# Optimization experiments

Hardware: AMD Instinct MI355X
Metric: run time of the kernel (lower is better)

Reference implementation:

```python
import jax, jax.numpy as jnp
import numpy as np

N_NODES = 100000


def _gcn_layer(x, src, dst, deg_inv_sqrt, W, b):
    # GCNConv: out = D^{-1/2} (A + I) D^{-1/2} X W + b  (symmetric norm, self-loops)
    xw = x @ W  # [N, out]
    norm = deg_inv_sqrt[src] * deg_inv_sqrt[dst]  # [E]
    msg = xw[src] * norm[:, None]  # [E, out] gathered messages
    agg = jax.ops.segment_sum(msg, dst, num_segments=N_NODES)
    # self-loop contribution: norm_ii = deg_inv_sqrt[i]^2
    agg = agg + (deg_inv_sqrt * deg_inv_sqrt)[:, None] * xw
    return agg + b


def setup_inputs() -> dict:
    key = jax.random.key(0)
    k1, k2, k3, k4, k5, k6 = jax.random.split(key, 6)
    F_IN, HID, OUT, E = 128, 256, 40, 1600000
    x = jax.random.normal(k1, (N_NODES, F_IN), dtype=jnp.float32)
    edge_index = jax.random.randint(k2, (2, E), 0, N_NODES, dtype=jnp.int64)
    s1 = 1.0 / np.sqrt(F_IN)
    s2 = 1.0 / np.sqrt(HID)
    W1 = jax.random.uniform(k3, (F_IN, HID), jnp.float32, -s1, s1)
    b1 = jnp.zeros((HID,), jnp.float32)
    W2 = jax.random.uniform(k4, (HID, OUT), jnp.float32, -s2, s2)
    b2 = jnp.zeros((OUT,), jnp.float32)
    return {"x": x, "edge_index": edge_index, "W1": W1, "b1": b1, "W2": W2, "b2": b2}


def reference(x, edge_index, W1, b1, W2, b2):
    src, dst = edge_index[0], edge_index[1]
    # degree with self-loops (GCNConv default add_self_loops=True)
    deg = jax.ops.segment_sum(jnp.ones_like(dst, dtype=x.dtype), dst, num_segments=N_NODES) + 1.0
    deg_inv_sqrt = jax.lax.rsqrt(deg)
    h = _gcn_layer(x, src, dst, deg_inv_sqrt, W1, b1)
    h = jax.nn.relu(h)
    # dropout is identity in eval mode
    h = _gcn_layer(h, src, dst, deg_inv_sqrt, W2, b2)
    return jax.nn.log_softmax(h, axis=1)
```

## Files before the change

kernel.cpp:

```cpp
#include <hip/hip_runtime.h>
#include <math.h>

typedef long long ll;
typedef unsigned int uint;
typedef __attribute__((ext_vector_type(8))) short bf16x8;
typedef __attribute__((ext_vector_type(4))) float f32x4;

#define FIN 128
#define HID 256
#define FOUT 40
#define NG 8
#define NBIN 64

__device__ __forceinline__ float bflo(uint u) { return __uint_as_float(u << 16); }
__device__ __forceinline__ float bfhi(uint u) { return __uint_as_float(u & 0xFFFF0000u); }
__device__ __forceinline__ unsigned short f2bf(float f) {
  uint u = __float_as_uint(f);
  u += 0x7FFFu + ((u >> 16) & 1u);
  return (unsigned short)(u >> 16);
}

__device__ __forceinline__ int detect64(const uint* __restrict__ ei) {
  return (ei[1] == 0u && ei[3] == 0u && ei[5] == 0u && ei[7] == 0u) ? 1 : 0;
}

__global__ __launch_bounds__(256) void k_init(
    const void* __restrict__ ei, int* __restrict__ cnt,
    const float* __restrict__ W1, const float* __restrict__ W2,
    unsigned short* __restrict__ w1p, unsigned short* __restrict__ w2p,
    int2* __restrict__ pairs, ll E) {
  int i = blockIdx.x * 256 + threadIdx.x;
  int T = gridDim.x * 256;
  if (i < 32768) {
    int j = i & 7, g = (i >> 3) & 3, c = (i >> 5) & 255, s = i >> 13;
    int k = s * 32 + g * 8 + j;
    w1p[i] = f2bf(W1[(size_t)k * HID + c]);
  } else if (i < 32768 + 12288) {
    int i2 = i - 32768;
    int j = i2 & 7, g = (i2 >> 3) & 3, q = i2 >> 5;
    int c = q % 48, s = q / 48;
    int k = s * 32 + g * 8 + j;
    w2p[i2] = (c < FOUT) ? f2bf(W2[(size_t)k * FOUT + c]) : (unsigned short)0;
  }
  int is64 = detect64((const uint*)ei);
  for (ll base = (ll)i * 4; base < E; base += (ll)T * 4) {
    int m = (int)((E - base < 4) ? (E - base) : 4);
    int s[4], d[4];
    if (is64) {
      if (m == 4) {
        longlong2 a0 = *(const longlong2*)((const ll*)ei + base);
        longlong2 a1 = *(const longlong2*)((const ll*)ei + base + 2);
        longlong2 b0 = *(const longlong2*)((const ll*)ei + E + base);
        longlong2 b1 = *(const longlong2*)((const ll*)ei + E + base + 2);
        s[0]=(int)a0.x; s[1]=(int)a0.y; s[2]=(int)a1.x; s[3]=(int)a1.y;
        d[0]=(int)b0.x; d[1]=(int)b0.y; d[2]=(int)b1.x; d[3]=(int)b1.y;
      } else {
        for (int j = 0; j < m; ++j) { s[j]=(int)((const ll*)ei)[base+j]; d[j]=(int)((const ll*)ei)[E+base+j]; }
      }
    } else {
      if (m == 4) {
        int4 a = *(const int4*)((const int*)ei + base);
        int4 b = *(const int4*)((const int*)ei + E + base);
        s[0]=a.x; s[1]=a.y; s[2]=a.z; s[3]=a.w;
        d[0]=b.x; d[1]=b.y; d[2]=b.z; d[3]=b.w;
      } else {
        for (int j = 0; j < m; ++j) { s[j]=((const int*)ei)[base+j]; d[j]=((const int*)ei)[E+base+j]; }
      }
    }
    if (m == 4) {
      *(int4*)(pairs + base)     = make_int4(s[0], d[0], s[1], d[1]);
      *(int4*)(pairs + base + 2) = make_int4(s[2], d[2], s[3], d[3]);
    } else {
      for (int j = 0; j < m; ++j) pairs[base + j] = make_int2(s[j], d[j]);
    }
    for (int j = 0; j < m; ++j) atomicAdd(&cnt[d[j]], 1);
  }
}

__global__ __launch_bounds__(1024) void k_scan1(const int* __restrict__ cnt,
                                                int* __restrict__ row_off,
                                                int* __restrict__ blksums, int n) {
  __shared__ int sm[1024];
  int t = threadIdx.x;
  int base = blockIdx.x * 4096 + t * 4;
  int v0 = (base + 0 < n) ? cnt[base + 0] : 0;
  int v1 = (base + 1 < n) ? cnt[base + 1] : 0;
  int v2 = (base + 2 < n) ? cnt[base + 2] : 0;
  int v3 = (base + 3 < n) ? cnt[base + 3] : 0;
  int s = v0 + v1 + v2 + v3;
  sm[t] = s;
  __syncthreads();
  for (int off = 1; off < 1024; off <<= 1) {
    int u = (t >= off) ? sm[t - off] : 0;
    __syncthreads();
    sm[t] += u;
    __syncthreads();
  }
  int excl = sm[t] - s;
  if (base + 0 < n) row_off[base + 0] = excl;
  if (base + 1 < n) row_off[base + 1] = excl + v0;
  if (base + 2 < n) row_off[base + 2] = excl + v0 + v1;
  if (base + 3 < n) row_off[base + 3] = excl + v0 + v1 + v2;
  if (t == 1023) blksums[blockIdx.x] = sm[1023];
}

__global__ void k_scan2(int* __restrict__ blksums, int nb) {
  if (threadIdx.x == 0 && blockIdx.x == 0) {
    int acc = 0;
    for (int i = 0; i < nb; ++i) { int v = blksums[i]; blksums[i] = acc; acc += v; }
    blksums[nb] = acc;
  }
}

__global__ __launch_bounds__(1024) void k_scan3(
    int* __restrict__ row_off, int* __restrict__ cursor,
    const int* __restrict__ blksums, float* __restrict__ dis,
    int* __restrict__ hist, int n, int nb) {
  __shared__ int lh[NBIN];
  int t = threadIdx.x;
  if (t < NBIN) lh[t] = 0;
  __syncthreads();
  int i = blockIdx.x * 1024 + t;
  if (i < n) {
    int c = cursor[i];
    int v = row_off[i] + blksums[i >> 12];
    row_off[i] = v;
    cursor[i] = v;
    dis[i] = rsqrtf((float)c + 1.0f);
    atomicAdd(&lh[min(c, NBIN - 1)], 1);
  }
  if (i == 0) row_off[n] = blksums[nb];
  __syncthreads();
  if (t < NBIN && lh[t]) atomicAdd(&hist[t], lh[t]);
}

__global__ void k_binpfx(const int* __restrict__ hist, int* __restrict__ bincur) {
  if (threadIdx.x == 0 && blockIdx.x == 0) {
    int acc = 0;
    for (int b = 0; b < NBIN; ++b) { int v = hist[b]; bincur[b] = acc; acc += v; }
  }
}

__global__ __launch_bounds__(256) void k_perm(
    const int* __restrict__ row_off, int* __restrict__ bincur,
    int* __restrict__ perm, int n) {
  __shared__ int lh[NBIN], lbase[NBIN];
  int t = threadIdx.x;
  if (t < NBIN) lh[t] = 0;
  __syncthreads();
  int base = blockIdx.x * 4096 + t * 16;
  int deg[16];
  #pragma unroll
  for (int j = 0; j < 16; ++j) {
    int i = base + j;
    if (i < n) {
      deg[j] = min(row_off[i + 1] - row_off[i], NBIN - 1);
      atomicAdd(&lh[deg[j]], 1);
    } else deg[j] = -1;
  }
  __syncthreads();
  if (t < NBIN) {
    lbase[t] = lh[t] ? atomicAdd(&bincur[t], lh[t]) : 0;
    lh[t] = 0;
  }
  __syncthreads();
  #pragma unroll
  for (int j = 0; j < 16; ++j) {
    if (deg[j] >= 0) {
      int r = atomicAdd(&lh[deg[j]], 1);
      perm[lbase[deg[j]] + r] = base + j;
    }
  }
}

__global__ __launch_bounds__(256) void k_fill(
    const int2* __restrict__ pairs, int* __restrict__ cursor,
    int* __restrict__ csr, ll E, int range, int n) {
  int g = blockIdx.x & (NG - 1);
  int lo = g * range;
  int hi = min(n, lo + range);
  ll tig = (ll)(blockIdx.x >> 3) * 256 + threadIdx.x;
  ll TIG = (ll)(gridDim.x >> 3) * 256;
  for (ll i = tig * 2; i < E; i += TIG * 2) {
    if (i + 1 < E) {
      int4 p = *(const int4*)(pairs + i);
      if (p.y >= lo && p.y < hi) { int pos = atomicAdd(&cursor[p.y], 1); csr[pos] = p.x; }
      if (p.w >= lo && p.w < hi) { int pos = atomicAdd(&cursor[p.w], 1); csr[pos] = p.z; }
    } else {
      int2 p = pairs[i];
      if (p.y >= lo && p.y < hi) { int pos = atomicAdd(&cursor[p.y], 1); csr[pos] = p.x; }
    }
  }
}

__global__ __launch_bounds__(256) void k_xcast(
    const float* __restrict__ x, const float* __restrict__ dis,
    unsigned short* __restrict__ xb, int total8) {
  int i = blockIdx.x * 256 + threadIdx.x;
  if (i >= total8) return;
  float w = dis[i >> 4];
  const float4* p = (const float4*)x + (size_t)i * 2;
  float4 a = p[0], b = p[1];
  uint4 o;
  o.x = (uint)f2bf(w * a.x) | ((uint)f2bf(w * a.y) << 16);
  o.y = (uint)f2bf(w * a.z) | ((uint)f2bf(w * a.w) << 16);
  o.z = (uint)f2bf(w * b.x) | ((uint)f2bf(w * b.y) << 16);
  o.w = (uint)f2bf(w * b.z) | ((uint)f2bf(w * b.w) << 16);
  *(uint4*)(xb + (size_t)i * 8) = o;
}

__device__ __forceinline__ void add8(float* a, uint4 r) {
  a[0] += bflo(r.x); a[1] += bfhi(r.x);
  a[2] += bflo(r.y); a[3] += bfhi(r.y);
  a[4] += bflo(r.z); a[5] += bfhi(r.z);
  a[6] += bflo(r.w); a[7] += bfhi(r.w);
}

__global__ __launch_bounds__(256) void k_fused1(
    const unsigned short* __restrict__ xb, const int* __restrict__ csr,
    const int* __restrict__ row_off, const float* __restrict__ dis,
    const int* __restrict__ perm,
    const unsigned short* __restrict__ w1p, const float* __restrict__ b1,
    const unsigned short* __restrict__ w2p, unsigned short* __restrict__ xw2b,
    int n)
{
  __shared__ __align__(16) unsigned short xsb[16 * 136];
  __shared__ __align__(16) unsigned short hsb[16 * 264];
  __shared__ int   nid[16];
  __shared__ float dsh[16];

  int tid = threadIdx.x;
  int n0 = blockIdx.x * 16;
  int wv = tid >> 6, lane = tid & 63, qq = lane >> 4, l16 = lane & 15;
  int nl = wv * 4 + qq;
  int idx = n0 + nl;
  int node = (idx < n) ? perm[idx] : -1;

  float a[8] = {0, 0, 0, 0, 0, 0, 0, 0};
  float di = 0.f;
  if (node >= 0) {
    di = dis[node];
    uint4 v = *((const uint4*)(xb + (size_t)node * FIN) + l16);
    add8(a, v);
    int e0 = row_off[node], e1 = row_off[node + 1];
    int e = e0;
    for (; e + 8 <= e1; e += 8) {
      int s0 = csr[e],     s1 = csr[e + 1], s2 = csr[e + 2], s3 = csr[e + 3];
      int s4 = csr[e + 4], s5 = csr[e + 5], s6 = csr[e + 6], s7 = csr[e + 7];
      uint4 r0 = *((const uint4*)(xb + (size_t)s0 * FIN) + l16);
      uint4 r1 = *((const uint4*)(xb + (size_t)s1 * FIN) + l16);
      uint4 r2 = *((const uint4*)(xb + (size_t)s2 * FIN) + l16);
      uint4 r3 = *((const uint4*)(xb + (size_t)s3 * FIN) + l16);
      uint4 r4 = *((const uint4*)(xb + (size_t)s4 * FIN) + l16);
      uint4 r5 = *((const uint4*)(xb + (size_t)s5 * FIN) + l16);
      uint4 r6 = *((const uint4*)(xb + (size_t)s6 * FIN) + l16);
      uint4 r7 = *((const uint4*)(xb + (size_t)s7 * FIN) + l16);
      add8(a, r0); add8(a, r1); add8(a, r2); add8(a, r3);
      add8(a, r4); add8(a, r5); add8(a, r6); add8(a, r7);
    }
    for (; e < e1; ++e) {
      uint4 r0 = *((const uint4*)(xb + (size_t)csr[e] * FIN) + l16);
      add8(a, r0);
    }
  }
  if (l16 == 0) { nid[nl] = node; dsh[nl] = di; }
  {
    uint4 pk;
    pk.x = (uint)f2bf(di * a[0]) | ((uint)f2bf(di * a[1]) << 16);
    pk.y = (uint)f2bf(di * a[2]) | ((uint)f2bf(di * a[3]) << 16);
    pk.z = (uint)f2bf(di * a[4]) | ((uint)f2bf(di * a[5]) << 16);
    pk.w = (uint)f2bf(di * a[6]) | ((uint)f2bf(di * a[7]) << 16);
    *(uint4*)(xsb + nl * 136 + l16 * 8) = pk;
  }
  __syncthreads();

  int mrow = lane & 15, g = lane >> 4;
  f32x4 acc1[4] = {{0,0,0,0},{0,0,0,0},{0,0,0,0},{0,0,0,0}};
  #pragma unroll
  for (int s = 0; s < 4; ++s) {
    bf16x8 av = *(const bf16x8*)(xsb + mrow * 136 + s * 32 + g * 8);
    #pragma unroll
    for (int t = 0; t < 4; ++t) {
      int c = wv * 64 + t * 16 + mrow;
      bf16x8 bv = *(const bf16x8*)(w1p + (((size_t)(s * 256 + c) * 4 + g) << 3));
      acc1[t] = __builtin_amdgcn_mfma_f32_16x16x32_bf16(av, bv, acc1[t], 0, 0, 0);
    }
  }
  #pragma unroll
  for (int t = 0; t < 4; ++t) {
    int c = wv * 64 + t * 16 + mrow;
    float bb = b1[c];
    #pragma unroll
    for (int r = 0; r < 4; ++r) {
      float v = fmaxf(acc1[t][r] + bb, 0.f);
      hsb[(g * 4 + r) * 264 + c] = f2bf(v);
    }
  }
  __syncthreads();

  if (wv < 3) {
    f32x4 acc2 = {0, 0, 0, 0};
    int c2 = wv * 16 + mrow;
    #pragma unroll
    for (int s = 0; s < 8; ++s) {
      bf16x8 av = *(const bf16x8*)(hsb + mrow * 264 + s * 32 + g * 8);
      bf16x8 bv = *(const bf16x8*)(w2p + (((size_t)(s * 48 + c2) * 4 + g) << 3));
      acc2 = __builtin_amdgcn_mfma_f32_16x16x32_bf16(av, bv, acc2, 0, 0, 0);
    }
    if (c2 < FOUT) {
      #pragma unroll
      for (int r = 0; r < 4; ++r) {
        int nodeg = nid[g * 4 + r];
        if (nodeg >= 0)
          xw2b[(size_t)nodeg * FOUT + c2] = f2bf(acc2[r] * dsh[g * 4 + r]);
      }
    }
  }
}

__global__ __launch_bounds__(256) void k_layer2(
    const unsigned short* __restrict__ xw2b, const int* __restrict__ csr,
    const int* __restrict__ row_off, const float* __restrict__ dis,
    const int* __restrict__ perm,
    const float* __restrict__ b2, float* __restrict__ out, int n)
{
  int tid = threadIdx.x;
  int idx = blockIdx.x * 16 + (tid >> 4);
  int l16 = tid & 15;
  if (idx >= n) return;
  int node = perm[idx];
  float di = dis[node];
  bool act = (l16 < 10);
  float a0 = 0.f, a1 = 0.f, a2 = 0.f, a3 = 0.f;
  if (act) {
    uint2 v = *((const uint2*)(xw2b + (size_t)node * FOUT) + l16);
    a0 = bflo(v.x); a1 = bfhi(v.x); a2 = bflo(v.y); a3 = bfhi(v.y);
  }
  int e0 = row_off[node], e1 = row_off[node + 1];
  int e = e0;
  for (; e + 8 <= e1; e += 8) {
    int s0 = csr[e],     s1 = csr[e + 1], s2 = csr[e + 2], s3 = csr[e + 3];
    int s4 = csr[e + 4], s5 = csr[e + 5], s6 = csr[e + 6], s7 = csr[e + 7];
    if (act) {
      uint2 r0 = *((const uint2*)(xw2b + (size_t)s0 * FOUT) + l16);
      uint2 r1 = *((const uint2*)(xw2b + (size_t)s1 * FOUT) + l16);
      uint2 r2 = *((const uint2*)(xw2b + (size_t)s2 * FOUT) + l16);
      uint2 r3 = *((const uint2*)(xw2b + (size_t)s3 * FOUT) + l16);
      uint2 r4 = *((const uint2*)(xw2b + (size_t)s4 * FOUT) + l16);
      uint2 r5 = *((const uint2*)(xw2b + (size_t)s5 * FOUT) + l16);
      uint2 r6 = *((const uint2*)(xw2b + (size_t)s6 * FOUT) + l16);
      uint2 r7 = *((const uint2*)(xw2b + (size_t)s7 * FOUT) + l16);
      a0 += bflo(r0.x); a1 += bfhi(r0.x); a2 += bflo(r0.y); a3 += bfhi(r0.y);
      a0 += bflo(r1.x); a1 += bfhi(r1.x); a2 += bflo(r1.y); a3 += bfhi(r1.y);
      a0 += bflo(r2.x); a1 += bfhi(r2.x); a2 += bflo(r2.y); a3 += bfhi(r2.y);
      a0 += bflo(r3.x); a1 += bfhi(r3.x); a2 += bflo(r3.y); a3 += bfhi(r3.y);
      a0 += bflo(r4.x); a1 += bfhi(r4.x); a2 += bflo(r4.y); a3 += bfhi(r4.y);
      a0 += bflo(r5.x); a1 += bfhi(r5.x); a2 += bflo(r5.y); a3 += bfhi(r5.y);
      a0 += bflo(r6.x); a1 += bfhi(r6.x); a2 += bflo(r6.y); a3 += bfhi(r6.y);
      a0 += bflo(r7.x); a1 += bfhi(r7.x); a2 += bflo(r7.y); a3 += bfhi(r7.y);
    }
  }
  for (; e < e1; ++e) {
    int s0 = csr[e];
    if (act) {
      uint2 r0 = *((const uint2*)(xw2b + (size_t)s0 * FOUT) + l16);
      a0 += bflo(r0.x); a1 += bfhi(r0.x); a2 += bflo(r0.y); a3 += bfhi(r0.y);
    }
  }
  float l0 = -INFINITY, l1 = -INFINITY, l2 = -INFINITY, l3 = -INFINITY;
  if (act) {
    float4 bv = *(const float4*)(b2 + l16 * 4);
    l0 = di * a0 + bv.x; l1 = di * a1 + bv.y;
    l2 = di * a2 + bv.z; l3 = di * a3 + bv.w;
  }
  float m = fmaxf(fmaxf(l0, l1), fmaxf(l2, l3));
  #pragma unroll
  for (int off = 8; off > 0; off >>= 1) m = fmaxf(m, __shfl_xor(m, off));
  float s = 0.f;
  if (act) s = expf(l0 - m) + expf(l1 - m) + expf(l2 - m) + expf(l3 - m);
  #pragma unroll
  for (int off = 8; off > 0; off >>= 1) s += __shfl_xor(s, off);
  if (act) {
    float ls = m + logf(s);
    float4 o = make_float4(l0 - ls, l1 - ls, l2 - ls, l3 - ls);
    *(float4*)(out + (size_t)node * FOUT + l16 * 4) = o;
  }
}

extern "C" void kernel_launch(void* const* d_in, const int* in_sizes, int n_in,
                              void* d_out, int out_size, void* d_ws, size_t ws_size,
                              hipStream_t stream) {
  const float* x  = (const float*)d_in[0];
  const void*  ei = d_in[1];
  const float* W1 = (const float*)d_in[2];
  const float* b1 = (const float*)d_in[3];
  const float* W2 = (const float*)d_in[4];
  const float* b2 = (const float*)d_in[5];
  float* out = (float*)d_out;

  int n = in_sizes[0] / FIN;
  ll  E = (ll)in_sizes[1] / 2;
  int nb = (n + 4095) / 4096;
  int range = (n + NG - 1) / NG;

  char* ws = (char*)d_ws;
  size_t off = 0;
  auto carve = [&](size_t bytes) -> char* {
    char* p = ws + off;
    off = (off + bytes + 255) & ~(size_t)255;
    return p;
  };
  int*   row_off = (int*)carve((size_t)(n + 1) * 4);
  int*   cursor  = (int*)carve((size_t)n * 4);
  int2*  pairs   = (int2*)carve((size_t)E * 8);
  int*   csr     = (int*)carve((size_t)E * 4);
  int*   blksums = (int*)carve(64 * 4);
  int*   hist    = (int*)carve(NBIN * 4);
  int*   bincur  = (int*)carve(NBIN * 4);
  int*   perm    = (int*)carve((size_t)n * 4);
  float* dis     = (float*)carve((size_t)n * 4);
  unsigned short* xb   = (unsigned short*)carve((size_t)n * FIN * 2);
  unsigned short* w1p  = (unsigned short*)carve(32768 * 2);
  unsigned short* w2p  = (unsigned short*)carve(12288 * 2);
  unsigned short* xw2b = (unsigned short*)carve((size_t)n * FOUT * 2);
  (void)n_in; (void)out_size; (void)ws_size;

  int gx8  = (n * FIN / 8 + 255) / 256;
  int gt16 = (n + 15) / 16;
  int gperm = (n + 4095) / 4096;

  hipMemsetAsync(cursor, 0, (size_t)n * 4, stream);
  hipMemsetAsync(hist, 0, NBIN * 4, stream);

  hipLaunchKernelGGL(k_init,  dim3(2048), dim3(256), 0, stream,
                     ei, cursor, W1, W2, w1p, w2p, pairs, E);
  hipLaunchKernelGGL(k_scan1, dim3(nb), dim3(1024), 0, stream, cursor, row_off, blksums, n);
  hipLaunchKernelGGL(k_scan2, dim3(1), dim3(1), 0, stream, blksums, nb);
  hipLaunchKernelGGL(k_scan3, dim3((n + 1023) / 1024), dim3(1024), 0, stream,
                     row_off, cursor, blksums, dis, hist, n, nb);
  hipLaunchKernelGGL(k_binpfx, dim3(1), dim3(1), 0, stream, hist, bincur);
  hipLaunchKernelGGL(k_perm,  dim3(gperm), dim3(256), 0, stream, row_off, bincur, perm, n);
  hipLaunchKernelGGL(k_fill,  dim3(2048), dim3(256), 0, stream, pairs, cursor, csr, E, range, n);
  hipLaunchKernelGGL(k_xcast, dim3(gx8), dim3(256), 0, stream, x, dis, xb, n * FIN / 8);
  hipLaunchKernelGGL(k_fused1, dim3(gt16), dim3(256), 0, stream,
                     xb, csr, row_off, dis, perm, w1p, b1, w2p, xw2b, n);
  hipLaunchKernelGGL(k_layer2, dim3(gt16), dim3(256), 0, stream,
                     xw2b, csr, row_off, dis, perm, b2, out, n);
}
```

Before: 300.9 us.

## Split degree counting into range-partitioned pass and reverse block order in aggregation kernels

Degree counting moves out of k_init into a new k_count kernel. It re-reads the packed pairs and does its atomics only on destination nodes in one of two ranges per block group, so atomic traffic stays localized in cache. The fill kernel's partition count drops from 8 to 2. The fused layer-1 and layer-2 kernels now walk blocks in reverse order, so the highest-degree nodes in the permutation start first (load-balance tail). The cost is one extra kernel launch and a second full pass over the pairs array.

```diff
diff --git a/kernel.cpp b/kernel.cpp
--- a/kernel.cpp
+++ b/kernel.cpp
@@ -9,7 +9,7 @@
 #define FIN 128
 #define HID 256
 #define FOUT 40
-#define NG 8
+#define NGF 2
 #define NBIN 64
 
 __device__ __forceinline__ float bflo(uint u) { return __uint_as_float(u << 16); }
@@ -25,7 +25,7 @@
 }
 
 __global__ __launch_bounds__(256) void k_init(
-    const void* __restrict__ ei, int* __restrict__ cnt,
+    const void* __restrict__ ei,
     const float* __restrict__ W1, const float* __restrict__ W2,
     unsigned short* __restrict__ w1p, unsigned short* __restrict__ w2p,
     int2* __restrict__ pairs, ll E) {
@@ -73,7 +73,25 @@
     } else {
       for (int j = 0; j < m; ++j) pairs[base + j] = make_int2(s[j], d[j]);
     }
-    for (int j = 0; j < m; ++j) atomicAdd(&cnt[d[j]], 1);
+  }
+}
+
+__global__ __launch_bounds__(256) void k_count(
+    const int2* __restrict__ pairs, int* __restrict__ cnt, ll E, int range, int n) {
+  int g = blockIdx.x & (NGF - 1);
+  int lo = g * range;
+  int hi = min(n, lo + range);
+  ll tig = (ll)(blockIdx.x >> 1) * 256 + threadIdx.x;
+  ll TIG = (ll)(gridDim.x >> 1) * 256;
+  for (ll i = tig * 2; i < E; i += TIG * 2) {
+    if (i + 1 < E) {
+      int4 p = *(const int4*)(pairs + i);
+      if (p.y >= lo && p.y < hi) atomicAdd(&cnt[p.y], 1);
+      if (p.w >= lo && p.w < hi) atomicAdd(&cnt[p.w], 1);
+    } else {
+      int2 p = pairs[i];
+      if (p.y >= lo && p.y < hi) atomicAdd(&cnt[p.y], 1);
+    }
   }
 }
 
@@ -176,11 +194,11 @@
 __global__ __launch_bounds__(256) void k_fill(
     const int2* __restrict__ pairs, int* __restrict__ cursor,
     int* __restrict__ csr, ll E, int range, int n) {
-  int g = blockIdx.x & (NG - 1);
+  int g = blockIdx.x & (NGF - 1);
   int lo = g * range;
   int hi = min(n, lo + range);
-  ll tig = (ll)(blockIdx.x >> 3) * 256 + threadIdx.x;
-  ll TIG = (ll)(gridDim.x >> 3) * 256;
+  ll tig = (ll)(blockIdx.x >> 1) * 256 + threadIdx.x;
+  ll TIG = (ll)(gridDim.x >> 1) * 256;
   for (ll i = tig * 2; i < E; i += TIG * 2) {
     if (i + 1 < E) {
       int4 p = *(const int4*)(pairs + i);
@@ -230,7 +248,7 @@
   __shared__ float dsh[16];
 
   int tid = threadIdx.x;
-  int n0 = blockIdx.x * 16;
+  int n0 = (gridDim.x - 1 - blockIdx.x) * 16;
   int wv = tid >> 6, lane = tid & 63, qq = lane >> 4, l16 = lane & 15;
   int nl = wv * 4 + qq;
   int idx = n0 + nl;
@@ -325,7 +343,7 @@
     const float* __restrict__ b2, float* __restrict__ out, int n)
 {
   int tid = threadIdx.x;
-  int idx = blockIdx.x * 16 + (tid >> 4);
+  int idx = (gridDim.x - 1 - blockIdx.x) * 16 + (tid >> 4);
   int l16 = tid & 15;
   if (idx >= n) return;
   int node = perm[idx];
@@ -401,7 +419,7 @@
   int n = in_sizes[0] / FIN;
   ll  E = (ll)in_sizes[1] / 2;
   int nb = (n + 4095) / 4096;
-  int range = (n + NG - 1) / NG;
+  int range = (n + NGF - 1) / NGF;
 
   char* ws = (char*)d_ws;
   size_t off = 0;
@@ -433,7 +451,8 @@
   hipMemsetAsync(hist, 0, NBIN * 4, stream);
 
   hipLaunchKernelGGL(k_init,  dim3(2048), dim3(256), 0, stream,
-                     ei, cursor, W1, W2, w1p, w2p, pairs, E);
+                     ei, W1, W2, w1p, w2p, pairs, E);
+  hipLaunchKernelGGL(k_count, dim3(2048), dim3(256), 0, stream, pairs, cursor, E, range, n);
   hipLaunchKernelGGL(k_scan1, dim3(nb), dim3(1024), 0, stream, cursor, row_off, blksums, n);
   hipLaunchKernelGGL(k_scan2, dim3(1), dim3(1), 0, stream, blksums, nb);
   hipLaunchKernelGGL(k_scan3, dim3((n + 1023) / 1024), dim3(1024), 0, stream,
```

New measurement: 356.7 us. 18.5% more time.

## Pre-partition edges by destination range in init, then count and fill per partition

Applied to the files above, without the earlier changes.

k_init now buckets edges into NG destination-range partitions via shared-memory histogram and global cursor, writing pairs into per-partition buffers instead of a flat array and dropping the global degree atomics. A new k_count kernel computes degrees from the partitioned buffers, and k_fill reads only its own partition instead of scanning all edges 8 times with a range filter. This cuts the redundant reads of the pair array and localizes atomics, at the cost of an extra kernel pass and a fixed per-partition capacity that silently drops edges if a partition overflows. Fused1 and layer2 also reverse block order so the perm-sorted heavy nodes are scheduled differently.

```diff
diff --git a/kernel.cpp b/kernel.cpp
--- a/kernel.cpp
+++ b/kernel.cpp
@@ -11,6 +11,7 @@
 #define FOUT 40
 #define NG 8
 #define NBIN 64
+#define CAPPAD 65536
 
 __device__ __forceinline__ float bflo(uint u) { return __uint_as_float(u << 16); }
 __device__ __forceinline__ float bfhi(uint u) { return __uint_as_float(u & 0xFFFF0000u); }
@@ -25,12 +26,14 @@
 }
 
 __global__ __launch_bounds__(256) void k_init(
-    const void* __restrict__ ei, int* __restrict__ cnt,
+    const void* __restrict__ ei,
     const float* __restrict__ W1, const float* __restrict__ W2,
     unsigned short* __restrict__ w1p, unsigned short* __restrict__ w2p,
-    int2* __restrict__ pairs, ll E) {
-  int i = blockIdx.x * 256 + threadIdx.x;
-  int T = gridDim.x * 256;
+    int2* __restrict__ partbuf, int* __restrict__ pcur,
+    ll E, int range, ll cap) {
+  __shared__ int lh[NG], lbase[NG];
+  int t = threadIdx.x;
+  int i = blockIdx.x * 256 + t;
   if (i < 32768) {
     int j = i & 7, g = (i >> 3) & 3, c = (i >> 5) & 255, s = i >> 13;
     int k = s * 32 + g * 8 + j;
@@ -42,10 +45,15 @@
     int k = s * 32 + g * 8 + j;
     w2p[i2] = (c < FOUT) ? f2bf(W2[(size_t)k * FOUT + c]) : (unsigned short)0;
   }
+  if (t < NG) lh[t] = 0;
+  __syncthreads();
+
   int is64 = detect64((const uint*)ei);
-  for (ll base = (ll)i * 4; base < E; base += (ll)T * 4) {
-    int m = (int)((E - base < 4) ? (E - base) : 4);
-    int s[4], d[4];
+  ll base = (ll)i * 4;
+  int m = 0;
+  int s[4], d[4], p[4], r[4];
+  if (base < E) {
+    m = (int)((E - base < 4) ? (E - base) : 4);
     if (is64) {
       if (m == 4) {
         longlong2 a0 = *(const longlong2*)((const ll*)ei + base);
@@ -67,13 +75,30 @@
         for (int j = 0; j < m; ++j) { s[j]=((const int*)ei)[base+j]; d[j]=((const int*)ei)[E+base+j]; }
       }
     }
-    if (m == 4) {
-      *(int4*)(pairs + base)     = make_int4(s[0], d[0], s[1], d[1]);
-      *(int4*)(pairs + base + 2) = make_int4(s[2], d[2], s[3], d[3]);
-    } else {
-      for (int j = 0; j < m; ++j) pairs[base + j] = make_int2(s[j], d[j]);
-    }
-    for (int j = 0; j < m; ++j) atomicAdd(&cnt[d[j]], 1);
+    for (int j = 0; j < m; ++j) {
+      p[j] = d[j] / range;
+      r[j] = atomicAdd(&lh[p[j]], 1);
+    }
+  }
+  __syncthreads();
+  if (t < NG) lbase[t] = lh[t] ? atomicAdd(&pcur[t], lh[t]) : 0;
+  __syncthreads();
+  for (int j = 0; j < m; ++j) {
+    ll slot = (ll)lbase[p[j]] + r[j];
+    if (slot < cap) partbuf[(ll)p[j] * cap + slot] = make_int2(s[j], d[j]);
+  }
+}
+
+__global__ __launch_bounds__(256) void k_count(
+    const int2* __restrict__ partbuf, const int* __restrict__ pcur,
+    int* __restrict__ cnt, ll cap) {
+  int g = blockIdx.x & (NG - 1);
+  const int2* pb = partbuf + (ll)g * cap;
+  int cnt_g = min(pcur[g], (int)cap);
+  int bg = blockIdx.x >> 3, NB = gridDim.x >> 3;
+  for (int i = bg * 256 + threadIdx.x; i < cnt_g; i += NB * 256) {
+    int2 p = pb[i];
+    atomicAdd(&cnt[p.y], 1);
   }
 }
 
@@ -174,22 +199,16 @@
 }
 
 __global__ __launch_bounds__(256) void k_fill(
-    const int2* __restrict__ pairs, int* __restrict__ cursor,
-    int* __restrict__ csr, ll E, int range, int n) {
+    const int2* __restrict__ partbuf, const int* __restrict__ pcur,
+    int* __restrict__ cursor, int* __restrict__ csr, ll cap) {
   int g = blockIdx.x & (NG - 1);
-  int lo = g * range;
-  int hi = min(n, lo + range);
-  ll tig = (ll)(blockIdx.x >> 3) * 256 + threadIdx.x;
-  ll TIG = (ll)(gridDim.x >> 3) * 256;
-  for (ll i = tig * 2; i < E; i += TIG * 2) {
-    if (i + 1 < E) {
-      int4 p = *(const int4*)(pairs + i);
-      if (p.y >= lo && p.y < hi) { int pos = atomicAdd(&cursor[p.y], 1); csr[pos] = p.x; }
-      if (p.w >= lo && p.w < hi) { int pos = atomicAdd(&cursor[p.w], 1); csr[pos] = p.z; }
-    } else {
-      int2 p = pairs[i];
-      if (p.y >= lo && p.y < hi) { int pos = atomicAdd(&cursor[p.y], 1); csr[pos] = p.x; }
-    }
+  const int2* pb = partbuf + (ll)g * cap;
+  int cnt_g = min(pcur[g], (int)cap);
+  int bg = blockIdx.x >> 3, NB = gridDim.x >> 3;
+  for (int i = bg * 256 + threadIdx.x; i < cnt_g; i += NB * 256) {
+    int2 p = pb[i];
+    int pos = atomicAdd(&cursor[p.y], 1);
+    csr[pos] = p.x;
   }
 }
 
@@ -230,7 +249,7 @@
   __shared__ float dsh[16];
 
   int tid = threadIdx.x;
-  int n0 = blockIdx.x * 16;
+  int n0 = (gridDim.x - 1 - blockIdx.x) * 16;
   int wv = tid >> 6, lane = tid & 63, qq = lane >> 4, l16 = lane & 15;
   int nl = wv * 4 + qq;
   int idx = n0 + nl;
@@ -325,7 +344,7 @@
     const float* __restrict__ b2, float* __restrict__ out, int n)
 {
   int tid = threadIdx.x;
-  int idx = blockIdx.x * 16 + (tid >> 4);
+  int idx = (gridDim.x - 1 - blockIdx.x) * 16 + (tid >> 4);
   int l16 = tid & 15;
   if (idx >= n) return;
   int node = perm[idx];
@@ -402,6 +421,7 @@
   ll  E = (ll)in_sizes[1] / 2;
   int nb = (n + 4095) / 4096;
   int range = (n + NG - 1) / NG;
+  ll  cap = E / NG + CAPPAD;
 
   char* ws = (char*)d_ws;
   size_t off = 0;
@@ -412,7 +432,8 @@
   };
   int*   row_off = (int*)carve((size_t)(n + 1) * 4);
   int*   cursor  = (int*)carve((size_t)n * 4);
-  int2*  pairs   = (int2*)carve((size_t)E * 8);
+  int2*  partbuf = (int2*)carve((size_t)NG * cap * 8);
+  int*   pcur    = (int*)carve(NG * 4);
   int*   csr     = (int*)carve((size_t)E * 4);
   int*   blksums = (int*)carve(64 * 4);
   int*   hist    = (int*)carve(NBIN * 4);
@@ -425,22 +446,25 @@
   unsigned short* xw2b = (unsigned short*)carve((size_t)n * FOUT * 2);
   (void)n_in; (void)out_size; (void)ws_size;
 
-  int gx8  = (n * FIN / 8 + 255) / 256;
-  int gt16 = (n + 15) / 16;
+  int gx8   = (n * FIN / 8 + 255) / 256;
+  int gt16  = (n + 15) / 16;
   int gperm = (n + 4095) / 4096;
+  int ginit = (int)((E + 1023) / 1024);
 
   hipMemsetAsync(cursor, 0, (size_t)n * 4, stream);
   hipMemsetAsync(hist, 0, NBIN * 4, stream);
-
-  hipLaunchKernelGGL(k_init,  dim3(2048), dim3(256), 0, stream,
-                     ei, cursor, W1, W2, w1p, w2p, pairs, E);
+  hipMemsetAsync(pcur, 0, NG * 4, stream);
+
+  hipLaunchKernelGGL(k_init,  dim3(ginit), dim3(256), 0, stream,
+                     ei, W1, W2, w1p, w2p, partbuf, pcur, E, range, cap);
+  hipLaunchKernelGGL(k_count, dim3(2048), dim3(256), 0, stream, partbuf, pcur, cursor, cap);
   hipLaunchKernelGGL(k_scan1, dim3(nb), dim3(1024), 0, stream, cursor, row_off, blksums, n);
   hipLaunchKernelGGL(k_scan2, dim3(1), dim3(1), 0, stream, blksums, nb);
   hipLaunchKernelGGL(k_scan3, dim3((n + 1023) / 1024), dim3(1024), 0, stream,
                      row_off, cursor, blksums, dis, hist, n, nb);
   hipLaunchKernelGGL(k_binpfx, dim3(1), dim3(1), 0, stream, hist, bincur);
   hipLaunchKernelGGL(k_perm,  dim3(gperm), dim3(256), 0, stream, row_off, bincur, perm, n);
-  hipLaunchKernelGGL(k_fill,  dim3(2048), dim3(256), 0, stream, pairs, cursor, csr, E, range, n);
+  hipLaunchKernelGGL(k_fill,  dim3(2048), dim3(256), 0, stream, partbuf, pcur, cursor, csr, cap);
   hipLaunchKernelGGL(k_xcast, dim3(gx8), dim3(256), 0, stream, x, dis, xb, n * FIN / 8);
   hipLaunchKernelGGL(k_fused1, dim3(gt16), dim3(256), 0, stream,
                      xb, csr, row_off, dis, perm, w1p, b1, w2p, xw2b, n);
```

After: 328.3 us. +9.1%, slower.
